# Kernel optimization log

Measured on AMD Instinct MI355X. Metric: run time of the kernel, lower is better.

## Reference

```python
import jax, jax.numpy as jnp
import numpy as np

B, N, R, L = 32768, 9, 128, 2
F = 4 * R  # ffn hidden
EPS = 1e-5


def setup_inputs() -> dict:
    key = jax.random.key(0)
    ks = jax.random.split(key, 12)
    graph = jax.random.uniform(ks[0], (B, N, N), dtype=jnp.float32)  # weighted adjacency
    op_idx = jax.random.randint(ks[1], (B, N), 0, 7)
    op_table = jax.random.normal(ks[2], (7, R), dtype=jnp.float32)
    dev_embed = jax.random.normal(ks[3], (1, R), dtype=jnp.float32)
    s = 1.0 / np.sqrt(R)
    gcn_W = jax.random.normal(ks[4], (L, R, R), dtype=jnp.float32) * s
    gcn_b = jnp.zeros((L, R), dtype=jnp.float32)
    ln_g = jnp.ones((L, R), dtype=jnp.float32)
    ln_b = jnp.zeros((L, R), dtype=jnp.float32)
    ffn_W1 = jax.random.normal(ks[5], (L, R, F), dtype=jnp.float32) * s
    ffn_b1 = jnp.zeros((L, F), dtype=jnp.float32)
    ffn_W2 = jax.random.normal(ks[6], (L, F, R), dtype=jnp.float32) * (1.0 / np.sqrt(F))
    ffn_b2 = jnp.zeros((L, R), dtype=jnp.float32)
    fc_w = jax.random.normal(ks[7], (R, 1), dtype=jnp.float32) * s
    fc_b = jnp.zeros((1,), dtype=jnp.float32)
    return dict(graph=graph, op_idx=op_idx, op_table=op_table, dev_embed=dev_embed,
                gcn_W=gcn_W, gcn_b=gcn_b, ln_g=ln_g, ln_b=ln_b,
                ffn_W1=ffn_W1, ffn_b1=ffn_b1, ffn_W2=ffn_W2, ffn_b2=ffn_b2,
                fc_w=fc_w, fc_b=fc_b)


def _layer_norm(x, g, b):
    mu = x.mean(-1, keepdims=True)
    var = ((x - mu) ** 2).mean(-1, keepdims=True)
    return (x - mu) * jax.lax.rsqrt(var + EPS) * g + b


def reference(graph, op_idx, op_table, dev_embed, gcn_W, gcn_b, ln_g, ln_b,
              ffn_W1, ffn_b1, ffn_W2, ffn_b2, fc_w, fc_b):
    # embedding lookup + broadcast-add of device embedding: [B, N, R]
    x = op_table[op_idx].reshape(B * N, R) + dev_embed
    x = x.reshape(B, N, R)
    # symmetric GCN normalization with self loops on the 9x9 adjacency
    a_hat = graph + jnp.eye(N, dtype=graph.dtype)[None]
    d_is = jax.lax.rsqrt(a_hat.sum(-1))  # [B, N]
    norm_adj = a_hat * d_is[:, :, None] * d_is[:, None, :]  # [B, N, N]
    for l in range(L):
        # message passing + linear
        h = jnp.einsum('bij,bjr->bir', norm_adj, x) @ gcn_W[l] + gcn_b[l]
        h = jax.nn.relu(h)
        h = _layer_norm(h, ln_g[l], ln_b[l])
        # residual FFN
        h = h + jax.nn.relu(h @ ffn_W1[l] + ffn_b1[l]) @ ffn_W2[l] + ffn_b2[l]
        x = h
    pooled = x.mean(axis=1)  # [B, R] readout over the 9 nodes
    y = jax.nn.sigmoid(pooled @ fc_w + fc_b).squeeze(-1)  # [B]
    return y
```

## Files before the change

kernel.cpp:

```cpp
#include <hip/hip_runtime.h>
#include <math.h>

#define NN 9
#define RR 128
#define FF 512
#define LL 2
#define GPB 7
#define ROWS 63

typedef __attribute__((ext_vector_type(8))) short bf16x8;
typedef __attribute__((ext_vector_type(4))) float f32x4;

__device__ __forceinline__ float4 ld4(const float* p) { return *reinterpret_cast<const float4*>(p); }
__device__ __forceinline__ float2 ld2(const float* p) { return *reinterpret_cast<const float2*>(p); }
__device__ __forceinline__ void st4(float* p, const float4 v) { *reinterpret_cast<float4*>(p) = v; }

__device__ __forceinline__ ushort f2bf(float f) {
    unsigned u = __float_as_uint(f);
    return (ushort)((u + 0x7fffu + ((u >> 16) & 1u)) >> 16);
}
__device__ __forceinline__ float bf2f(ushort h) { return __uint_as_float(((unsigned)h) << 16); }

__device__ __forceinline__ void async16(void* lds, const void* g) {
    __builtin_amdgcn_global_load_lds(
        (const __attribute__((address_space(1))) unsigned int*)g,
        (__attribute__((address_space(3))) unsigned int*)lds,
        16, 0, 0);
}

#define SWZ(row, c) ((row) * 128 + ((c) ^ (((row) & 7) << 3)))

__global__ __launch_bounds__(256)
void pack_weights(const float* __restrict__ gcn_W,
                  const float* __restrict__ ffn_W1,
                  const float* __restrict__ ffn_W2,
                  ushort* __restrict__ wsw)
{
    const int t    = blockIdx.x * 256 + threadIdx.x;
    const int lane = t & 63;
    const int slot = t >> 6;
    const int grp  = lane >> 4, cl = lane & 15;

    const float* src; int ldn, kbase, n;
    if (slot < 64) {
        const int l = slot >> 5, ks = (slot >> 3) & 3, nt = slot & 7;
        src = gcn_W + l * RR * RR; ldn = RR;
        kbase = ks * 32 + grp * 8;
        n = nt * 16 + cl;
    } else if (slot < 320) {
        const int s = slot - 64;
        const int l = s >> 7, p = (s >> 5) & 3, ks = (s >> 3) & 3, nt = s & 7;
        src = ffn_W1 + l * RR * FF; ldn = FF;
        kbase = ks * 32 + grp * 8;
        n = p * 128 + nt * 16 + cl;
    } else {
        const int s = slot - 320;
        const int l = s >> 7, p = (s >> 5) & 3, ks = (s >> 3) & 3, nt = s & 7;
        src = ffn_W2 + l * FF * RR; ldn = RR;
        kbase = p * 128 + ks * 32 + grp * 8;
        n = nt * 16 + cl;
    }
    ushort v[8];
    #pragma unroll
    for (int j = 0; j < 8; ++j) v[j] = f2bf(src[(size_t)(kbase + j) * ldn + n]);
    uint4 o;
    o.x = v[0] | ((unsigned)v[1] << 16);
    o.y = v[2] | ((unsigned)v[3] << 16);
    o.z = v[4] | ((unsigned)v[5] << 16);
    o.w = v[6] | ((unsigned)v[7] << 16);
    *reinterpret_cast<uint4*>(wsw + ((size_t)slot * 64 + lane) * 8) = o;
}

__device__ __forceinline__ int g16(int l, int kh)         { return (l * 4 + kh * 2) * 8; }
__device__ __forceinline__ int w1g(int l, int p, int kh)  { return 64 + ((l * 4 + p) * 4 + kh * 2) * 8; }
__device__ __forceinline__ int w2g(int l, int p, int kh)  { return 320 + ((l * 4 + p) * 4 + kh * 2) * 8; }

#define MMA22(T, SRCARR, KH, BUFSEL)                                           \
    {                                                                          \
        const unsigned char* bb_ = &wbuf[BUFSEL][lane << 4];                   \
        _Pragma("unroll")                                                      \
        for (int ki = 0; ki < 2; ++ki) {                                       \
            const bf16x8 a0_ = *(const bf16x8*)&SRCARR[SWZ(rh32 + cl,          \
                                        ((KH) * 2 + ki) * 32 + grp * 8)];      \
            const bf16x8 a1_ = *(const bf16x8*)&SRCARR[SWZ(rh32 + 16 + cl,     \
                                        ((KH) * 2 + ki) * 32 + grp * 8)];      \
            _Pragma("unroll")                                                  \
            for (int nt = 0; nt < 4; ++nt) {                                   \
                const bf16x8 b_ = *(const bf16x8*)(bb_ +                       \
                                        ((ki * 8 + ch4 + nt) << 10));          \
                T[nt]     = __builtin_amdgcn_mfma_f32_16x16x32_bf16(a0_, b_, T[nt], 0, 0, 0);     \
                T[4 + nt] = __builtin_amdgcn_mfma_f32_16x16x32_bf16(a1_, b_, T[4 + nt], 0, 0, 0); \
            }                                                                  \
        }                                                                      \
    }

#define STAGE16(DST, FRAGBASE)                                                 \
    {                                                                          \
        const unsigned char* g_ = wsb + ((size_t)((FRAGBASE) + ms * 4) << 10)  \
                                      + (lane << 4);                           \
        async16(&wbuf[DST][(ms * 4 + 0) << 10], g_);                           \
        async16(&wbuf[DST][(ms * 4 + 1) << 10], g_ + 1024);                    \
        async16(&wbuf[DST][(ms * 4 + 2) << 10], g_ + 2048);                    \
        async16(&wbuf[DST][(ms * 4 + 3) << 10], g_ + 3072);                    \
    }

__global__ __launch_bounds__(256, 2)
void backbone_mfma(const float* __restrict__ graph,
                   const int*   __restrict__ op_idx,
                   const float* __restrict__ op_table,
                   const float* __restrict__ dev_embed,
                   const float* __restrict__ gcn_b,
                   const float* __restrict__ ln_g,
                   const float* __restrict__ ln_b,
                   const float* __restrict__ ffn_b1,
                   const float* __restrict__ ffn_b2,
                   const float* __restrict__ fc_w,
                   const float* __restrict__ fc_b,
                   const ushort* __restrict__ wsw,
                   float* __restrict__ out,
                   const int nB)
{
    __shared__ alignas(16) ushort sA[64 * 128];
    __shared__ alignas(16) ushort sGH[64 * 128];
    __shared__ float sNA[GPB][81];
    __shared__ float sD[ROWS];
    __shared__ float2 sLN[64][2];
    __shared__ float sRD[64][2];
    __shared__ alignas(16) unsigned char wbuf[2][16384];

    const int tid  = threadIdx.x;
    const int lane = tid & 63;
    const int ms   = tid >> 6;
    const int grp  = lane >> 4;
    const int cl   = lane & 15;
    const int c0   = lane * 2;
    const int rh32 = (ms >> 1) * 32;
    const int ch4  = (ms & 1) * 4;
    const int cb   = ch4 * 16;
    const int R0   = ms * 16;
    const int b0   = blockIdx.x * GPB;

    const unsigned char* wsb = (const unsigned char*)wsw;

    if (tid < 64) {
        *reinterpret_cast<unsigned*>(&sA[SWZ(63, tid * 2)])  = 0u;
        *reinterpret_cast<unsigned*>(&sGH[SWZ(63, tid * 2)]) = 0u;
    }

    {
        const float2 dv = ld2(&dev_embed[c0]);
        #pragma unroll
        for (int rr = 0; rr < 16; ++rr) {
            const int row = R0 + rr;
            if (row < ROWS) {
                const int gi = row / NN, ni = row - gi * NN;
                const int gg = min(b0 + gi, nB - 1);
                const int idx = op_idx[gg * NN + ni];
                float2 v = ld2(&op_table[idx * RR + c0]);
                unsigned pk = f2bf(v.x + dv.x) | ((unsigned)f2bf(v.y + dv.y) << 16);
                *reinterpret_cast<unsigned*>(&sA[SWZ(row, c0)]) = pk;
            }
        }
    }

    for (int e = tid; e < GPB * 81; e += 256) {
        const int gi = e / 81, r = e - gi * 81;
        const int i = r / NN, j = r - i * NN;
        const int gg = min(b0 + gi, nB - 1);
        sNA[gi][r] = graph[(size_t)gg * 81 + r] + (i == j ? 1.0f : 0.0f);
    }
    __syncthreads();
    if (tid < ROWS) {
        const int gi = tid / NN, i = tid - gi * NN;
        float s = 0.f;
        #pragma unroll
        for (int j = 0; j < NN; ++j) s += sNA[gi][i * NN + j];
        sD[tid] = rsqrtf(s);
    }
    __syncthreads();
    for (int e = tid; e < GPB * 81; e += 256) {
        const int gi = e / 81, r = e - gi * 81;
        const int i = r / NN, j = r - i * NN;
        sNA[gi][r] *= sD[gi * NN + i] * sD[gi * NN + j];
    }

    int cur = 0;
    STAGE16(0, g16(0, 0));
    __syncthreads();

    f32x4 acc[8];

    for (int l = 0; l < LL; ++l) {
        {
            const int g0 = R0 / NN, g1 = (R0 + 15) / NN;
            for (int gi = g0; gi <= g1 && gi < GPB; ++gi) {
                float xr[2 * NN];
                #pragma unroll
                for (int j = 0; j < NN; ++j) {
                    unsigned u = *reinterpret_cast<const unsigned*>(&sA[SWZ(gi * NN + j, c0)]);
                    xr[2 * j]     = bf2f((ushort)(u & 0xffffu));
                    xr[2 * j + 1] = bf2f((ushort)(u >> 16));
                }
                const int rlo = max(R0, gi * NN), rhi = min(R0 + 16, gi * NN + NN);
                for (int row = rlo; row < rhi; ++row) {
                    const int ni = row - gi * NN;
                    float a0 = 0.f, a1 = 0.f;
                    #pragma unroll
                    for (int j = 0; j < NN; ++j) {
                        const float w = sNA[gi][ni * NN + j];
                        a0 = fmaf(w, xr[2 * j], a0);
                        a1 = fmaf(w, xr[2 * j + 1], a1);
                    }
                    unsigned pk = f2bf(a0) | ((unsigned)f2bf(a1) << 16);
                    *reinterpret_cast<unsigned*>(&sGH[SWZ(row, c0)]) = pk;
                }
            }
        }
        __syncthreads();

        #pragma unroll
        for (int i = 0; i < 8; ++i) acc[i] = (f32x4){0.f, 0.f, 0.f, 0.f};
        #pragma unroll
        for (int kh = 0; kh < 2; ++kh) {
            const int nb = (kh == 0) ? g16(l, 1) : w1g(l, 0, 0);
            STAGE16(cur ^ 1, nb);
            MMA22(acc, sGH, kh, cur);
            __syncthreads();
            cur ^= 1;
        }

        {
            float sv[8] = {0,0,0,0,0,0,0,0}, qv[8] = {0,0,0,0,0,0,0,0};
            #pragma unroll
            for (int rg = 0; rg < 2; ++rg) {
                #pragma unroll
                for (int nt = 0; nt < 4; ++nt) {
                    const float gb = gcn_b[l * RR + cb + nt * 16 + cl];
                    #pragma unroll
                    for (int r = 0; r < 4; ++r) {
                        float v = fmaxf(acc[rg * 4 + nt][r] + gb, 0.f);
                        acc[rg * 4 + nt][r] = v;
                        sv[rg * 4 + r] += v; qv[rg * 4 + r] += v * v;
                    }
                }
            }
            #pragma unroll
            for (int i = 0; i < 8; ++i) {
                #pragma unroll
                for (int m = 1; m <= 8; m <<= 1) {
                    sv[i] += __shfl_xor(sv[i], m);
                    qv[i] += __shfl_xor(qv[i], m);
                }
            }
            if (cl == 0) {
                #pragma unroll
                for (int rg = 0; rg < 2; ++rg)
                    #pragma unroll
                    for (int r = 0; r < 4; ++r)
                        sLN[rh32 + rg * 16 + grp * 4 + r][ms & 1] =
                            make_float2(sv[rg * 4 + r], qv[rg * 4 + r]);
            }
            __syncthreads();
            float mu[8], rs[8];
            #pragma unroll
            for (int rg = 0; rg < 2; ++rg) {
                #pragma unroll
                for (int r = 0; r < 4; ++r) {
                    const float2 a = sLN[rh32 + rg * 16 + grp * 4 + r][0];
                    const float2 b = sLN[rh32 + rg * 16 + grp * 4 + r][1];
                    const float s = a.x + b.x, q = a.y + b.y;
                    const float m_ = s * (1.f / RR);
                    mu[rg * 4 + r] = m_;
                    rs[rg * 4 + r] = rsqrtf(q * (1.f / RR) - m_ * m_ + 1e-5f);
                }
            }
            #pragma unroll
            for (int rg = 0; rg < 2; ++rg) {
                #pragma unroll
                for (int nt = 0; nt < 4; ++nt) {
                    const float lgv = ln_g[l * RR + cb + nt * 16 + cl];
                    const float lbv = ln_b[l * RR + cb + nt * 16 + cl];
                    #pragma unroll
                    for (int r = 0; r < 4; ++r)
                        acc[rg * 4 + nt][r] = (acc[rg * 4 + nt][r] - mu[rg * 4 + r])
                                              * rs[rg * 4 + r] * lgv + lbv;
                }
            }
        }

        #pragma unroll
        for (int rg = 0; rg < 2; ++rg)
            #pragma unroll
            for (int nt = 0; nt < 4; ++nt)
                #pragma unroll
                for (int r = 0; r < 4; ++r)
                    sA[SWZ(rh32 + rg * 16 + grp * 4 + r, cb + nt * 16 + cl)]
                        = f2bf(acc[rg * 4 + nt][r]);
        #pragma unroll
        for (int rg = 0; rg < 2; ++rg)
            #pragma unroll
            for (int nt = 0; nt < 4; ++nt) {
                const float b2v = ffn_b2[l * RR + cb + nt * 16 + cl];
                #pragma unroll
                for (int r = 0; r < 4; ++r) acc[rg * 4 + nt][r] += b2v;
            }
        __syncthreads();

        for (int p = 0; p < 4; ++p) {
            f32x4 t[8];
            #pragma unroll
            for (int rg = 0; rg < 2; ++rg)
                #pragma unroll
                for (int nt = 0; nt < 4; ++nt) {
                    const float b1v = ffn_b1[l * FF + p * 128 + cb + nt * 16 + cl];
                    t[rg * 4 + nt] = (f32x4){b1v, b1v, b1v, b1v};
                }
            #pragma unroll
            for (int kh = 0; kh < 2; ++kh) {
                const int nb = (kh == 0) ? w1g(l, p, 1) : w2g(l, p, 0);
                STAGE16(cur ^ 1, nb);
                MMA22(t, sA, kh, cur);
                __syncthreads();
                cur ^= 1;
            }
            #pragma unroll
            for (int rg = 0; rg < 2; ++rg)
                #pragma unroll
                for (int nt = 0; nt < 4; ++nt)
                    #pragma unroll
                    for (int r = 0; r < 4; ++r)
                        sGH[SWZ(rh32 + rg * 16 + grp * 4 + r, cb + nt * 16 + cl)]
                            = f2bf(fmaxf(t[rg * 4 + nt][r], 0.f));
            __syncthreads();
            #pragma unroll
            for (int kh = 0; kh < 2; ++kh) {
                const bool last = (l == LL - 1) && (p == 3) && (kh == 1);
                const int nb = (kh == 0) ? w2g(l, p, 1)
                             : ((p < 3) ? w1g(l, p + 1, 0) : g16(l + 1, 0));
                if (!last) STAGE16(cur ^ 1, nb);
                MMA22(acc, sGH, kh, cur);
                __syncthreads();
                cur ^= 1;
            }
        }

        if (l + 1 < LL) {
            #pragma unroll
            for (int rg = 0; rg < 2; ++rg)
                #pragma unroll
                for (int nt = 0; nt < 4; ++nt)
                    #pragma unroll
                    for (int r = 0; r < 4; ++r)
                        sA[SWZ(rh32 + rg * 16 + grp * 4 + r, cb + nt * 16 + cl)]
                            = f2bf(acc[rg * 4 + nt][r]);
            __syncthreads();
        }
    }

    {
        float p4[8] = {0,0,0,0,0,0,0,0};
        #pragma unroll
        for (int rg = 0; rg < 2; ++rg)
            #pragma unroll
            for (int nt = 0; nt < 4; ++nt) {
                const float fw = fc_w[cb + nt * 16 + cl];
                #pragma unroll
                for (int r = 0; r < 4; ++r)
                    p4[rg * 4 + r] = fmaf(acc[rg * 4 + nt][r], fw, p4[rg * 4 + r]);
            }
        #pragma unroll
        for (int i = 0; i < 8; ++i) {
            #pragma unroll
            for (int m = 1; m <= 8; m <<= 1) p4[i] += __shfl_xor(p4[i], m);
        }
        if (cl == 0) {
            #pragma unroll
            for (int rg = 0; rg < 2; ++rg)
                #pragma unroll
                for (int r = 0; r < 4; ++r)
                    sRD[rh32 + rg * 16 + grp * 4 + r][ms & 1] = p4[rg * 4 + r];
        }
        __syncthreads();
        if (tid < GPB) {
            const int g = b0 + tid;
            if (g < nB) {
                float s = 0.f;
                #pragma unroll
                for (int n = 0; n < NN; ++n)
                    s += sRD[tid * NN + n][0] + sRD[tid * NN + n][1];
                out[g] = 1.f / (1.f + expf(-(s * (1.f / 9.f) + fc_b[0])));
            }
        }
    }
}

__device__ __forceinline__ void fma4(float4& d, const float a, const float4 w) {
    d.x = fmaf(a, w.x, d.x); d.y = fmaf(a, w.y, d.y);
    d.z = fmaf(a, w.z, d.z); d.w = fmaf(a, w.w, d.w);
}
__device__ __forceinline__ void xadd32(float4& v) {
    v.x += __shfl_xor(v.x, 32); v.y += __shfl_xor(v.y, 32);
    v.z += __shfl_xor(v.z, 32); v.w += __shfl_xor(v.w, 32);
}
__device__ __forceinline__ void relu4f(float4& v) {
    v.x = fmaxf(v.x, 0.f); v.y = fmaxf(v.y, 0.f);
    v.z = fmaxf(v.z, 0.f); v.w = fmaxf(v.w, 0.f);
}

__global__ __launch_bounds__(256)
void backbone_fp32(const float* __restrict__ graph, const int* __restrict__ op_idx,
                   const float* __restrict__ op_table, const float* __restrict__ dev_embed,
                   const float* __restrict__ gcn_W, const float* __restrict__ gcn_b,
                   const float* __restrict__ ln_g, const float* __restrict__ ln_b,
                   const float* __restrict__ ffn_W1, const float* __restrict__ ffn_b1,
                   const float* __restrict__ ffn_W2, const float* __restrict__ ffn_b2,
                   const float* __restrict__ fc_w, const float* __restrict__ fc_b,
                   float* __restrict__ out)
{
    __shared__ float sX[4][NN][RR];
    __shared__ float sT[4][NN][RR];
    __shared__ float sNA[4][81];
    __shared__ float sD[4][NN];

    const int tid  = threadIdx.x;
    const int lane = tid & 63;
    const int cg   = tid & 31;
    const int half = (tid >> 5) & 1;
    const int ms   = tid >> 6;
    const int c0   = cg * 4;
    const int k0   = half * 64;
    const int g    = blockIdx.x * 4 + ms;

    {
        const float dv0 = dev_embed[lane];
        const float dv1 = dev_embed[lane + 64];
        #pragma unroll
        for (int j = 0; j < NN; ++j) {
            const int idx = op_idx[g * NN + j];
            sX[ms][j][lane]      = op_table[idx * RR + lane]      + dv0;
            sX[ms][j][lane + 64] = op_table[idx * RR + lane + 64] + dv1;
        }
    }
    {
        const float* gp = graph + (size_t)g * 81;
        { const int i = lane / NN, j = lane - i * NN;
          sNA[ms][lane] = gp[lane] + (i == j ? 1.0f : 0.0f); }
        if (lane < 17) { const int e = lane + 64; const int i = e / NN, j = e - i * NN;
          sNA[ms][e] = gp[e] + (i == j ? 1.0f : 0.0f); }
        if (lane < NN) {
            float s = 0.f;
            #pragma unroll
            for (int j = 0; j < NN; ++j) s += sNA[ms][lane * NN + j];
            sD[ms][lane] = rsqrtf(s);
        }
        { const int i = lane / NN, j = lane - i * NN; sNA[ms][lane] *= sD[ms][i] * sD[ms][j]; }
        if (lane < 17) { const int e = lane + 64; const int i = e / NN, j = e - i * NN;
          sNA[ms][e] *= sD[ms][i] * sD[ms][j]; }
    }

    float4 acc[NN];
    for (int l = 0; l < LL; ++l) {
        const float* gw = gcn_W  + l * RR * RR;
        const float* gb = gcn_b  + l * RR;
        const float* lg = ln_g   + l * RR;
        const float* lb = ln_b   + l * RR;
        const float* w1 = ffn_W1 + l * RR * FF;
        const float* b1 = ffn_b1 + l * FF;
        const float* w2 = ffn_W2 + l * FF * RR;
        const float* b2 = ffn_b2 + l * RR;
        {
            float4 xv[NN];
            #pragma unroll
            for (int j = 0; j < NN; ++j) xv[j] = ld4(&sX[ms][j][c0]);
            #pragma unroll
            for (int ii = 0; ii < 5; ++ii) {
                const int i = ii + half * 5;
                if (i < NN) {
                    float4 a = make_float4(0.f, 0.f, 0.f, 0.f);
                    #pragma unroll
                    for (int j = 0; j < NN; ++j) fma4(a, sNA[ms][i * NN + j], xv[j]);
                    st4(&sT[ms][i][c0], a);
                }
            }
        }
        float4 h[NN];
        {
            const float4 z4 = make_float4(0.f, 0.f, 0.f, 0.f);
            const float4 gbv = ld4(&gb[c0]);
            const float4 ini = half ? z4 : gbv;
            #pragma unroll
            for (int i = 0; i < NN; ++i) h[i] = ini;
            #pragma unroll 2
            for (int kk = 0; kk < 64; kk += 4) {
                const float* wp = gw + (size_t)(k0 + kk) * RR + c0;
                const float4 wv0 = ld4(wp), wv1 = ld4(wp + RR), wv2 = ld4(wp + 2 * RR), wv3 = ld4(wp + 3 * RR);
                #pragma unroll
                for (int i = 0; i < NN; ++i) {
                    const float4 a = ld4(&sT[ms][i][k0 + kk]);
                    fma4(h[i], a.x, wv0); fma4(h[i], a.y, wv1);
                    fma4(h[i], a.z, wv2); fma4(h[i], a.w, wv3);
                }
            }
            #pragma unroll
            for (int i = 0; i < NN; ++i) xadd32(h[i]);
        }
        {
            const float4 lgv = ld4(&lg[c0]);
            const float4 lbv = ld4(&lb[c0]);
            #pragma unroll
            for (int i = 0; i < NN; ++i) {
                float4 v = h[i]; relu4f(v);
                float s = v.x + v.y + v.z + v.w;
                float q = v.x*v.x + v.y*v.y + v.z*v.z + v.w*v.w;
                #pragma unroll
                for (int m = 1; m <= 16; m <<= 1) { s += __shfl_xor(s, m); q += __shfl_xor(q, m); }
                const float mu = s * (1.f / RR);
                const float var = q * (1.f / RR) - mu * mu;
                const float rs = rsqrtf(var + 1e-5f);
                v.x = (v.x - mu) * rs * lgv.x + lbv.x;
                v.y = (v.y - mu) * rs * lgv.y + lbv.y;
                v.z = (v.z - mu) * rs * lgv.z + lbv.z;
                v.w = (v.w - mu) * rs * lgv.w + lbv.w;
                h[i] = v;
            }
        }
        #pragma unroll
        for (int i = 0; i < NN; ++i) st4(&sX[ms][i][c0], h[i]);
        {
            const float4 b2v = ld4(&b2[c0]);
            #pragma unroll
            for (int i = 0; i < NN; ++i) {
                if (half) acc[i] = make_float4(0.f, 0.f, 0.f, 0.f);
                else { acc[i] = h[i];
                       acc[i].x += b2v.x; acc[i].y += b2v.y; acc[i].z += b2v.z; acc[i].w += b2v.w; }
            }
        }
        for (int p = 0; p < 4; ++p) {
            const int f0 = p * RR + c0;
            float4 t[NN];
            {
                const float4 z4 = make_float4(0.f, 0.f, 0.f, 0.f);
                const float4 b1v = ld4(&b1[f0]);
                const float4 ini = half ? z4 : b1v;
                #pragma unroll
                for (int i = 0; i < NN; ++i) t[i] = ini;
            }
            #pragma unroll 2
            for (int kk = 0; kk < 64; kk += 4) {
                const float* wp = w1 + (size_t)(k0 + kk) * FF + f0;
                const float4 wv0 = ld4(wp), wv1 = ld4(wp + FF), wv2 = ld4(wp + 2 * FF), wv3 = ld4(wp + 3 * FF);
                #pragma unroll
                for (int i = 0; i < NN; ++i) {
                    const float4 a = ld4(&sX[ms][i][k0 + kk]);
                    fma4(t[i], a.x, wv0); fma4(t[i], a.y, wv1);
                    fma4(t[i], a.z, wv2); fma4(t[i], a.w, wv3);
                }
            }
            #pragma unroll
            for (int i = 0; i < NN; ++i) { xadd32(t[i]); relu4f(t[i]); st4(&sT[ms][i][c0], t[i]); }
            #pragma unroll 2
            for (int kk = 0; kk < 64; kk += 4) {
                const float* wp = w2 + (size_t)(p * RR + k0 + kk) * RR + c0;
                const float4 wv0 = ld4(wp), wv1 = ld4(wp + RR), wv2 = ld4(wp + 2 * RR), wv3 = ld4(wp + 3 * RR);
                #pragma unroll
                for (int i = 0; i < NN; ++i) {
                    const float4 a = ld4(&sT[ms][i][k0 + kk]);
                    fma4(acc[i], a.x, wv0); fma4(acc[i], a.y, wv1);
                    fma4(acc[i], a.z, wv2); fma4(acc[i], a.w, wv3);
                }
            }
        }
        #pragma unroll
        for (int i = 0; i < NN; ++i) xadd32(acc[i]);
        if (l + 1 < LL) {
            #pragma unroll
            for (int i = 0; i < NN; ++i) st4(&sX[ms][i][c0], acc[i]);
        }
    }
    {
        const float4 fw = ld4(&fc_w[c0]);
        float4 pv = make_float4(0.f, 0.f, 0.f, 0.f);
        #pragma unroll
        for (int i = 0; i < NN; ++i) { pv.x += acc[i].x; pv.y += acc[i].y; pv.z += acc[i].z; pv.w += acc[i].w; }
        float part = (pv.x*fw.x + pv.y*fw.y + pv.z*fw.z + pv.w*fw.w) * (1.f / 9.f);
        #pragma unroll
        for (int m = 1; m <= 16; m <<= 1) part += __shfl_xor(part, m);
        if (lane == 0) out[g] = 1.f / (1.f + expf(-(part + fc_b[0])));
    }
}

extern "C" void kernel_launch(void* const* d_in, const int* in_sizes, int n_in,
                              void* d_out, int out_size, void* d_ws, size_t ws_size,
                              hipStream_t stream) {
    const float* graph     = (const float*)d_in[0];
    const int*   op_idx    = (const int*)  d_in[1];
    const float* op_table  = (const float*)d_in[2];
    const float* dev_embed = (const float*)d_in[3];
    const float* gcn_W     = (const float*)d_in[4];
    const float* gcn_b     = (const float*)d_in[5];
    const float* ln_g      = (const float*)d_in[6];
    const float* ln_b      = (const float*)d_in[7];
    const float* ffn_W1    = (const float*)d_in[8];
    const float* ffn_b1    = (const float*)d_in[9];
    const float* ffn_W2    = (const float*)d_in[10];
    const float* ffn_b2    = (const float*)d_in[11];
    const float* fc_w      = (const float*)d_in[12];
    const float* fc_b      = (const float*)d_in[13];
    float* out = (float*)d_out;

    const int nB = in_sizes[0] / 81;
    const size_t WS_NEED = 576 * 1024;

    if (d_ws != nullptr && ws_size >= WS_NEED) {
        pack_weights<<<dim3(144), dim3(256), 0, stream>>>(gcn_W, ffn_W1, ffn_W2, (ushort*)d_ws);
        backbone_mfma<<<dim3((nB + GPB - 1) / GPB), dim3(256), 0, stream>>>(
            graph, op_idx, op_table, dev_embed, gcn_b, ln_g, ln_b,
            ffn_b1, ffn_b2, fc_w, fc_b, (const ushort*)d_ws, out, nB);
    } else {
        backbone_fp32<<<dim3(nB / 4), dim3(256), 0, stream>>>(
            graph, op_idx, op_table, dev_embed, gcn_W, gcn_b, ln_g, ln_b,
            ffn_W1, ffn_b1, ffn_W2, ffn_b2, fc_w, fc_b, out);
    }
}
```

Baseline: 389.7 us.

## Read packed weight fragments directly from global instead of double-buffered LDS staging

Removes the async global-to-LDS double-buffered staging of weight fragments and has each wave load its B fragments straight from global memory (L2-cached packed bf16) inside the MFMA loop. This drops the 32KB wbuf shared allocation and several __syncthreads per GEMM stage, which could raise occupancy and cut barrier overhead. In exchange, each wave issues its own global loads with latency exposed in the MFMA loop, and waves sharing the same column half fetch the same weights redundantly.

Result: no change. 388.4 us (-0.3%).

```diff
diff --git a/kernel.cpp b/kernel.cpp
--- a/kernel.cpp
+++ b/kernel.cpp
@@ -20,13 +20,6 @@
     return (ushort)((u + 0x7fffu + ((u >> 16) & 1u)) >> 16);
 }
 __device__ __forceinline__ float bf2f(ushort h) { return __uint_as_float(((unsigned)h) << 16); }
-
-__device__ __forceinline__ void async16(void* lds, const void* g) {
-    __builtin_amdgcn_global_load_lds(
-        (const __attribute__((address_space(1))) unsigned int*)g,
-        (__attribute__((address_space(3))) unsigned int*)lds,
-        16, 0, 0);
-}
 
 #define SWZ(row, c) ((row) * 128 + ((c) ^ (((row) & 7) << 3)))
 
@@ -71,37 +64,26 @@
     *reinterpret_cast<uint4*>(wsw + ((size_t)slot * 64 + lane) * 8) = o;
 }
 
-__device__ __forceinline__ int g16(int l, int kh)         { return (l * 4 + kh * 2) * 8; }
-__device__ __forceinline__ int w1g(int l, int p, int kh)  { return 64 + ((l * 4 + p) * 4 + kh * 2) * 8; }
-__device__ __forceinline__ int w2g(int l, int p, int kh)  { return 320 + ((l * 4 + p) * 4 + kh * 2) * 8; }
-
-#define MMA22(T, SRCARR, KH, BUFSEL)                                           \
+__device__ __forceinline__ int gcnF(int l)        { return l * 32; }
+__device__ __forceinline__ int w1F(int l, int p)  { return 64 + (l * 4 + p) * 32; }
+__device__ __forceinline__ int w2F(int l, int p)  { return 320 + (l * 4 + p) * 32; }
+
+#define MMA22G(T, SRCARR, FRAGBASE)                                            \
     {                                                                          \
-        const unsigned char* bb_ = &wbuf[BUFSEL][lane << 4];                   \
+        const bf16x8* bp_ = wb + (size_t)((FRAGBASE) + ch4) * 64 + lane;       \
         _Pragma("unroll")                                                      \
-        for (int ki = 0; ki < 2; ++ki) {                                       \
+        for (int ki = 0; ki < 4; ++ki) {                                       \
             const bf16x8 a0_ = *(const bf16x8*)&SRCARR[SWZ(rh32 + cl,          \
-                                        ((KH) * 2 + ki) * 32 + grp * 8)];      \
+                                        ki * 32 + grp * 8)];                   \
             const bf16x8 a1_ = *(const bf16x8*)&SRCARR[SWZ(rh32 + 16 + cl,     \
-                                        ((KH) * 2 + ki) * 32 + grp * 8)];      \
+                                        ki * 32 + grp * 8)];                   \
             _Pragma("unroll")                                                  \
             for (int nt = 0; nt < 4; ++nt) {                                   \
-                const bf16x8 b_ = *(const bf16x8*)(bb_ +                       \
-                                        ((ki * 8 + ch4 + nt) << 10));          \
+                const bf16x8 b_ = bp_[(ki * 8 + nt) * 64];                     \
                 T[nt]     = __builtin_amdgcn_mfma_f32_16x16x32_bf16(a0_, b_, T[nt], 0, 0, 0);     \
                 T[4 + nt] = __builtin_amdgcn_mfma_f32_16x16x32_bf16(a1_, b_, T[4 + nt], 0, 0, 0); \
             }                                                                  \
         }                                                                      \
-    }
-
-#define STAGE16(DST, FRAGBASE)                                                 \
-    {                                                                          \
-        const unsigned char* g_ = wsb + ((size_t)((FRAGBASE) + ms * 4) << 10)  \
-                                      + (lane << 4);                           \
-        async16(&wbuf[DST][(ms * 4 + 0) << 10], g_);                           \
-        async16(&wbuf[DST][(ms * 4 + 1) << 10], g_ + 1024);                    \
-        async16(&wbuf[DST][(ms * 4 + 2) << 10], g_ + 2048);                    \
-        async16(&wbuf[DST][(ms * 4 + 3) << 10], g_ + 3072);                    \
     }
 
 __global__ __launch_bounds__(256, 2)
@@ -126,7 +108,6 @@
     __shared__ float sD[ROWS];
     __shared__ float2 sLN[64][2];
     __shared__ float sRD[64][2];
-    __shared__ alignas(16) unsigned char wbuf[2][16384];
 
     const int tid  = threadIdx.x;
     const int lane = tid & 63;
@@ -140,7 +121,7 @@
     const int R0   = ms * 16;
     const int b0   = blockIdx.x * GPB;
 
-    const unsigned char* wsb = (const unsigned char*)wsw;
+    const bf16x8* wb = reinterpret_cast<const bf16x8*>(wsw);
 
     if (tid < 64) {
         *reinterpret_cast<unsigned*>(&sA[SWZ(63, tid * 2)])  = 0u;
@@ -183,9 +164,6 @@
         const int i = r / NN, j = r - i * NN;
         sNA[gi][r] *= sD[gi * NN + i] * sD[gi * NN + j];
     }
-
-    int cur = 0;
-    STAGE16(0, g16(0, 0));
     __syncthreads();
 
     f32x4 acc[8];
@@ -220,14 +198,7 @@
 
         #pragma unroll
         for (int i = 0; i < 8; ++i) acc[i] = (f32x4){0.f, 0.f, 0.f, 0.f};
-        #pragma unroll
-        for (int kh = 0; kh < 2; ++kh) {
-            const int nb = (kh == 0) ? g16(l, 1) : w1g(l, 0, 0);
-            STAGE16(cur ^ 1, nb);
-            MMA22(acc, sGH, kh, cur);
-            __syncthreads();
-            cur ^= 1;
-        }
+        MMA22G(acc, sGH, gcnF(l));
 
         {
             float sv[8] = {0,0,0,0,0,0,0,0}, qv[8] = {0,0,0,0,0,0,0,0};
@@ -315,14 +286,8 @@
                     const float b1v = ffn_b1[l * FF + p * 128 + cb + nt * 16 + cl];
                     t[rg * 4 + nt] = (f32x4){b1v, b1v, b1v, b1v};
                 }
-            #pragma unroll
-            for (int kh = 0; kh < 2; ++kh) {
-                const int nb = (kh == 0) ? w1g(l, p, 1) : w2g(l, p, 0);
-                STAGE16(cur ^ 1, nb);
-                MMA22(t, sA, kh, cur);
-                __syncthreads();
-                cur ^= 1;
-            }
+            MMA22G(t, sA, w1F(l, p));
+
             #pragma unroll
             for (int rg = 0; rg < 2; ++rg)
                 #pragma unroll
@@ -332,16 +297,10 @@
                         sGH[SWZ(rh32 + rg * 16 + grp * 4 + r, cb + nt * 16 + cl)]
                             = f2bf(fmaxf(t[rg * 4 + nt][r], 0.f));
             __syncthreads();
-            #pragma unroll
-            for (int kh = 0; kh < 2; ++kh) {
-                const bool last = (l == LL - 1) && (p == 3) && (kh == 1);
-                const int nb = (kh == 0) ? w2g(l, p, 1)
-                             : ((p < 3) ? w1g(l, p + 1, 0) : g16(l + 1, 0));
-                if (!last) STAGE16(cur ^ 1, nb);
-                MMA22(acc, sGH, kh, cur);
-                __syncthreads();
-                cur ^= 1;
-            }
+
+            MMA22G(acc, sGH, w2F(l, p));
+
+            if (p < 3) __syncthreads();
         }
 
         if (l + 1 < LL) {
```
